# Optimization experiments

Hardware: AMD Instinct MI355X
Metric: run time of the kernel (lower is better)

The kernel has to match this reference:

```python
import jax, jax.numpy as jnp
import numpy as np

B, CIN, H, W = 32, 16, 32, 128
COUT = 128


def _run_direction(x_hwbc, p):
    # x_hwbc: (H, W, B, CIN); scan order is raster (top-to-bottom, left-to-right).
    # Predecessors: dim0 = cell above (previous row), dim1 = cell to the left.
    xi = jnp.einsum('hwbc,oc->hwbo', x_hwbc, p['w_ii'])
    xf = jnp.einsum('hwbc,oc->hwbo', x_hwbc, p['w_if'])
    xg = jnp.einsum('hwbc,oc->hwbo', x_hwbc, p['w_ig'])
    xo = jnp.einsum('hwbc,oc->hwbo', x_hwbc, p['w_io'])
    Wdim, Bdim = x_hwbc.shape[1], x_hwbc.shape[2]
    O = p['w_hi'].shape[0]
    ws0, ws1 = p['ws'][0], p['ws'][1]

    def branch(xi_, xf_, xg_, xo_, c, h):
        i = jax.nn.sigmoid(xi_ + h @ p['w_hi'].T + p['b_i'])
        f = jax.nn.sigmoid(xf_ + h @ p['w_hf'].T + p['b_f'])
        g = jnp.tanh(xg_ + h @ p['w_hg'].T + p['b_g'])
        o = jax.nn.sigmoid(xo_ + h @ p['w_ho'].T + p['b_o'])
        cn = f * c + i * g
        return cn, o * jnp.tanh(cn)

    def col_step(carry, inp):
        c_left, h_left = carry                      # (B, O)
        xi_, xf_, xg_, xo_, c_top, h_top = inp      # each (B, O)
        c0, h0 = branch(xi_, xf_, xg_, xo_, c_top, h_top)   # vertical predecessor
        c1, h1 = branch(xi_, xf_, xg_, xo_, c_left, h_left) # horizontal predecessor
        ct = ws0 * c0 + ws1 * c1 + p['bias']
        ht = ws0 * h0 + ws1 * h1 + p['bias']
        return (ct, ht), (ct, ht)

    def row_step(carry, row):
        c_top, h_top = carry                        # (W, B, O)
        xi_r, xf_r, xg_r, xo_r = row
        z = jnp.zeros((Bdim, O), xi_r.dtype)
        _, (c_row, h_row) = jax.lax.scan(col_step, (z, z), (xi_r, xf_r, xg_r, xo_r, c_top, h_top))
        return (c_row, h_row), h_row

    z_row = jnp.zeros((Wdim, Bdim, O), x_hwbc.dtype)
    _, h_all = jax.lax.scan(row_step, (z_row, z_row), (xi, xf, xg, xo))
    return h_all  # (H, W, B, O)


def _forward(x, w_ii, w_hi, b_i, w_if, w_hf, b_f, w_ig, w_hg, b_g,
             w_io, w_ho, b_o, weighted_sum, bias):
    # Four scan directions realized by flipping the grid (lr_tb, rl_tb, lr_bt, rl_bt).
    x_hwbc = jnp.transpose(x, (2, 3, 0, 1))  # (H, W, B, CIN)
    flips = [(False, False), (False, True), (True, False), (True, True)]
    outs = []
    for d, (fy, fx) in enumerate(flips):
        xd = x_hwbc
        if fy:
            xd = xd[::-1]
        if fx:
            xd = xd[:, ::-1]
        p = {'w_ii': w_ii[d], 'w_hi': w_hi[d], 'b_i': b_i[d],
             'w_if': w_if[d], 'w_hf': w_hf[d], 'b_f': b_f[d],
             'w_ig': w_ig[d], 'w_hg': w_hg[d], 'b_g': b_g[d],
             'w_io': w_io[d], 'w_ho': w_ho[d], 'b_o': b_o[d],
             'ws': weighted_sum[d], 'bias': bias[d]}
        h = _run_direction(xd, p)
        if fy:
            h = h[::-1]
        if fx:
            h = h[:, ::-1]
        outs.append(h)
    h4 = jnp.stack(outs)                      # (4, H, W, B, O)
    return jnp.transpose(h4, (0, 4, 3, 1, 2)) # (4, O, B, H, W)


def setup_inputs() -> dict:
    key = jax.random.key(0)
    ks = jax.random.split(key, 16)
    xw = lambda k: jax.random.normal(k, (4, COUT, CIN), jnp.float32) * 0.05
    hw = lambda k: jax.random.normal(k, (4, COUT, COUT), jnp.float32) * 0.05
    bb = lambda k: jax.random.normal(k, (4, COUT), jnp.float32) * 0.05
    return {
        'x': jax.random.normal(ks[0], (B, CIN, H, W), jnp.float32),
        'w_ii': xw(ks[1]), 'w_hi': hw(ks[2]), 'b_i': bb(ks[3]),
        'w_if': xw(ks[4]), 'w_hf': hw(ks[5]), 'b_f': bb(ks[6]),
        'w_ig': xw(ks[7]), 'w_hg': hw(ks[8]), 'b_g': bb(ks[9]),
        'w_io': xw(ks[10]), 'w_ho': hw(ks[11]), 'b_o': bb(ks[12]),
        'weighted_sum': jax.random.uniform(ks[13], (4, 2), jnp.float32),
        'bias': bb(ks[14]),
    }


def reference(x, w_ii, w_hi, b_i, w_if, w_hf, b_f, w_ig, w_hg, b_g,
              w_io, w_ho, b_o, weighted_sum, bias):
    return _forward(x, w_ii, w_hi, b_i, w_if, w_hf, b_f, w_ig, w_hg, b_g,
                    w_io, w_ho, b_o, weighted_sum, bias)
```

## Files before the change

### kernel.cpp

```cpp
#include <hip/hip_runtime.h>

#define Hh 32
#define Ww 128
#define BB 32
#define CC 16
#define OO 128
#define DEPTH 4
#define SPIN_CAP (1 << 23)
#define FSTRIDE 32

typedef __attribute__((ext_vector_type(8))) short short8;
typedef __attribute__((ext_vector_type(4))) float f32x4;

__device__ inline short f2bf(float f) {
    unsigned u = __builtin_bit_cast(unsigned, f);
    unsigned r = (u + 0x7FFFu + ((u >> 16) & 1u)) >> 16;
    return (short)r;
}
__device__ inline float bf2f(short s) {
    unsigned u = ((unsigned)(unsigned short)s) << 16;
    return __builtin_bit_cast(float, u);
}
__device__ inline float rcp_(float x) { return __builtin_amdgcn_rcpf(x); }
__device__ inline float sigm(float x) {
    return rcp_(1.f + __builtin_amdgcn_exp2f(-1.442695041f * x));
}
__device__ inline float tanh_(float x) {
    return 1.f - 2.f * rcp_(__builtin_amdgcn_exp2f(2.885390082f * x) + 1.f);
}

__device__ inline unsigned long long aload64(const unsigned long long* p) {
    return __hip_atomic_load(p, __ATOMIC_RELAXED, __HIP_MEMORY_SCOPE_AGENT);
}
__device__ inline void astore64(unsigned long long* p, unsigned long long v) {
    __hip_atomic_store(p, v, __ATOMIC_RELAXED, __HIP_MEMORY_SCOPE_AGENT);
}
__device__ inline short aloadS(const short* p) {
    return __hip_atomic_load(p, __ATOMIC_RELAXED, __HIP_MEMORY_SCOPE_AGENT);
}
__device__ inline int aloadI(const int* p) {
    return __hip_atomic_load(p, __ATOMIC_RELAXED, __HIP_MEMORY_SCOPE_AGENT);
}
__device__ inline void astoreI(int* p, int v) {
    __hip_atomic_store(p, v, __ATOMIC_RELAXED, __HIP_MEMORY_SCOPE_AGENT);
}

__global__ void mdlstm_init(const float* __restrict__ x, short* __restrict__ xT,
                            int* __restrict__ flags) {
    int idx = blockIdx.x * 256 + threadIdx.x;
    if (blockIdx.x < 64) flags[idx] = 0;
    int w = idx & 127;
    int h = (idx >> 7) & 31;
    int c = (idx >> 12) & 15;
    int b = idx >> 16;
    float v = x[idx];
    xT[((h * Ww + w) * BB + b) * CC + c] = f2bf(v);
}

__global__ void __launch_bounds__(512, 1) mdlstm_main(
    const short* __restrict__ xT,
    const float* __restrict__ w_ii, const float* __restrict__ w_hi, const float* __restrict__ b_i,
    const float* __restrict__ w_if, const float* __restrict__ w_hf, const float* __restrict__ b_f,
    const float* __restrict__ w_ig, const float* __restrict__ w_hg, const float* __restrict__ b_g,
    const float* __restrict__ w_io, const float* __restrict__ w_ho, const float* __restrict__ b_o,
    const float* __restrict__ wsum, const float* __restrict__ bias,
    short* __restrict__ hring, float* __restrict__ cring,
    int* __restrict__ prog, int* __restrict__ cons,
    float* __restrict__ out)
{
    const int chain = blockIdx.x & 7;
    const int r     = blockIdx.x >> 3;
    const int d     = chain >> 1;
    const int s     = chain & 1;
    const int b0    = s * 16;
    const bool fy   = (d >= 2);
    const bool fx   = (d & 1);
    const int hh    = fy ? (Hh - 1 - r) : r;

    const int tid  = threadIdx.x;
    const int wv   = tid >> 6;
    const int lane = tid & 63;
    const int lr   = lane & 15;
    const int lh   = lane >> 4;
    const int on   = wv * 16 + lr;

    __shared__ short stage[OO * 256];

    const float* whp[4] = {w_hi, w_hf, w_hg, w_ho};
    const float* wip[4] = {w_ii, w_if, w_ig, w_io};
    short8 whf[4][4];
    short8 wif_[4];
#pragma unroll
    for (int g = 0; g < 4; ++g) {
#pragma unroll
        for (int kt = 0; kt < 4; ++kt) {
            const float* p = whp[g] + ((d * OO + on) * OO + kt * 32 + lh * 8);
            short8 f;
#pragma unroll
            for (int j = 0; j < 8; ++j) f[j] = f2bf(p[j]);
            whf[g][kt] = f;
        }
        short8 fi = (short8)(short)0;
        if (lh < 2) {
            const float* p = wip[g] + ((d * OO + on) * CC + lh * 8);
#pragma unroll
            for (int j = 0; j < 8; ++j) fi[j] = f2bf(p[j]);
        }
        wif_[g] = fi;
    }

    const float bi  = b_i[d * OO + on];
    const float bf_ = b_f[d * OO + on];
    const float bg_ = b_g[d * OO + on];
    const float bo_ = b_o[d * OO + on];
    const float bb_ = bias[d * OO + on];
    const float ws0 = wsum[d * 2 + 0];
    const float ws1 = wsum[d * 2 + 1];

    int* topf      = prog + ((d * 32 + (r - 1)) * 2 + s) * FSTRIDE;
    int* myprog    = prog + ((d * 32 + r) * 2 + s) * FSTRIDE;
    int* mycons    = cons + ((d * 32 + r) * 2 + s) * FSTRIDE;
    int* consnext  = cons + ((d * 32 + (r + 1)) * 2 + s) * FSTRIDE;

    const int rb_me  = (d * 32 + r) * DEPTH * BB * OO;
    const int rb_top = (d * 32 + (r - 1)) * DEPTH * BB * OO;

    short8 hLf[4];
#pragma unroll
    for (int kt = 0; kt < 4; ++kt) hLf[kt] = (short8)(short)0;
    float cL[4] = {0.f, 0.f, 0.f, 0.f};

    short8 hTfB[4];
#pragma unroll
    for (int kt = 0; kt < 4; ++kt) hTfB[kt] = (short8)(short)0;
    float cTB[4] = {0.f, 0.f, 0.f, 0.f};

    int top_seen = 0, cons_seen = 0;
    const f32x4 zacc = {0.f, 0.f, 0.f, 0.f};

#pragma unroll 2
    for (int wsc = 0; wsc < Ww; ++wsc) {
        const int ww    = fx ? (Ww - 1 - wsc) : wsc;
        const int slot  = wsc & (DEPTH - 1);
        const int wslot = ww & 15;
        const bool evenc = ((wsc & 1) == 0);

        short8 xf = (short8)(short)0;
        if (lh < 2) {
            const short* p = xT + ((hh * Ww + ww) * BB + b0 + lr) * CC + lh * 8;
            xf = *(const short8*)p;
        }

        short8 hTf[4];
        float cT[4];
        if (r > 0) {
            if (evenc) {
                const int need = wsc + 2;
                if (top_seen < need) {
                    int spin = 0;
                    while (top_seen < need && spin < SPIN_CAP) {
                        int v = 0;
                        if (lane == 0) v = aloadI(topf);
                        v = __shfl(v, 0, 64);
                        if (v < need) { __builtin_amdgcn_s_sleep(1); ++spin; } else top_seen = v;
                    }
                }
                const short* hb = hring + rb_top + slot * OO * BB + b0 + lr;
#pragma unroll
                for (int kt = 0; kt < 4; ++kt) {
                    short8 f;
#pragma unroll
                    for (int jj = 0; jj < 8; ++jj)
                        f[jj] = aloadS(hb + (kt * 32 + lh * 8 + jj) * BB);
                    hTf[kt] = f;
                }
                const short* hb2 = hb + OO * BB;
#pragma unroll
                for (int kt = 0; kt < 4; ++kt) {
                    short8 f;
#pragma unroll
                    for (int jj = 0; jj < 8; ++jj)
                        f[jj] = aloadS(hb2 + (kt * 32 + lh * 8 + jj) * BB);
                    hTfB[kt] = f;
                }
                const unsigned long long* cp =
                    (const unsigned long long*)(cring + rb_top + slot * OO * BB + on * BB + b0 + lh * 4);
                union { unsigned long long q; float f[2]; } c01, c23;
                c01.q = aload64(cp);
                c23.q = aload64(cp + 1);
                cT[0] = c01.f[0]; cT[1] = c01.f[1]; cT[2] = c23.f[0]; cT[3] = c23.f[1];
                const unsigned long long* cp2 = cp + (OO * BB / 2);
                c01.q = aload64(cp2);
                c23.q = aload64(cp2 + 1);
                cTB[0] = c01.f[0]; cTB[1] = c01.f[1]; cTB[2] = c23.f[0]; cTB[3] = c23.f[1];
            } else {
#pragma unroll
                for (int kt = 0; kt < 4; ++kt) hTf[kt] = hTfB[kt];
#pragma unroll
                for (int j = 0; j < 4; ++j) cT[j] = cTB[j];
            }
        } else {
#pragma unroll
            for (int kt = 0; kt < 4; ++kt) hTf[kt] = (short8)(short)0;
#pragma unroll
            for (int j = 0; j < 4; ++j) cT[j] = 0.f;
        }

        f32x4 ax[4], accL[4], accT[4];
#pragma unroll
        for (int g = 0; g < 4; ++g)
            ax[g] = __builtin_amdgcn_mfma_f32_16x16x32_bf16(xf, wif_[g], zacc, 0, 0, 0);
#pragma unroll
        for (int g = 0; g < 4; ++g) {
            f32x4 a = ax[g];
#pragma unroll
            for (int kt = 0; kt < 4; ++kt)
                a = __builtin_amdgcn_mfma_f32_16x16x32_bf16(hLf[kt], whf[g][kt], a, 0, 0, 0);
            accL[g] = a;
        }
#pragma unroll
        for (int g = 0; g < 4; ++g) {
            f32x4 a = ax[g];
#pragma unroll
            for (int kt = 0; kt < 4; ++kt)
                a = __builtin_amdgcn_mfma_f32_16x16x32_bf16(hTf[kt], whf[g][kt], a, 0, 0, 0);
            accT[g] = a;
        }

        float ctv[4];
        union { short sh[4]; unsigned long long q; } hpack;
#pragma unroll
        for (int j = 0; j < 4; ++j) {
            float iT = sigm(accT[0][j] + bi);
            float fT = sigm(accT[1][j] + bf_);
            float gT = tanh_(accT[2][j] + bg_);
            float oT = sigm(accT[3][j] + bo_);
            float c0 = fT * cT[j] + iT * gT;
            float h0 = oT * tanh_(c0);

            float iL = sigm(accL[0][j] + bi);
            float fL = sigm(accL[1][j] + bf_);
            float gL = tanh_(accL[2][j] + bg_);
            float oL = sigm(accL[3][j] + bo_);
            float c1 = fL * cL[j] + iL * gL;
            float h1 = oL * tanh_(c1);

            float ct = ws0 * c0 + ws1 * c1 + bb_;
            float ht = ws0 * h0 + ws1 * h1 + bb_;
            cL[j] = ct;
            ctv[j] = ct;
            hpack.sh[j] = f2bf(ht);
        }

        {
            const int g_on = (on >> 3) & 15;
            *(unsigned long long*)&stage[on * 256 + ((wslot ^ g_on) << 4) + lh * 4] = hpack.q;
        }

        if (r < 31 && evenc && wsc >= DEPTH) {
            const int need = wsc - 2;
            if (cons_seen < need) {
                int spin = 0;
                while (cons_seen < need && spin < SPIN_CAP) {
                    int v = 0;
                    if (lane == 0) v = aloadI(consnext);
                    v = __shfl(v, 0, 64);
                    if (v < need) { __builtin_amdgcn_s_sleep(1); ++spin; } else cons_seen = v;
                }
            }
        }

        if (r < 31) {
            astore64((unsigned long long*)(hring + rb_me + slot * OO * BB + on * BB + b0 + lh * 4),
                     hpack.q);
            union { float f[2]; unsigned long long q; } p01, p23;
            p01.f[0] = ctv[0]; p01.f[1] = ctv[1];
            p23.f[0] = ctv[2]; p23.f[1] = ctv[3];
            unsigned long long* cp =
                (unsigned long long*)(cring + rb_me + slot * OO * BB + on * BB + b0 + lh * 4);
            astore64(cp, p01.q);
            astore64(cp + 1, p23.q);
        }

        __syncthreads();

        if (!evenc && tid == 0) {
            if (r < 31) astoreI(myprog, wsc + 1);
            if (r > 0)  astoreI(mycons, wsc + 1);
        }

        if (r > 0 && !evenc && wsc < Ww - 1) {
            int v = 0;
            if (lane == 0) v = aloadI(topf);
            v = __shfl(v, 0, 64);
            if (v > top_seen) top_seen = v;
        }

#pragma unroll
        for (int kt = 0; kt < 4; ++kt) {
            const int col = ((wslot ^ (kt * 4 + lh)) << 4) + lr;
            short8 f;
#pragma unroll
            for (int jj = 0; jj < 8; ++jj)
                f[jj] = stage[(kt * 32 + lh * 8 + jj) * 256 + col];
            hLf[kt] = f;
        }

        if ((wsc & 15) == 15) {
            const int wbase = ww & ~15;
            const int q  = tid & 3;
            const int r0 = tid >> 2;
#pragma unroll
            for (int i = 0; i < 16; ++i) {
                const int row = r0 + (i << 7);
                const int o = row >> 4;
                const int b = row & 15;
                const int go = (o >> 3) & 15;
                f32x4 v;
#pragma unroll
                for (int k = 0; k < 4; ++k)
                    v[k] = bf2f(stage[o * 256 + (((q * 4 + k) ^ go) << 4) + b]);
                float* op = out + ((size_t)((d * OO + o) * BB + b0 + b)) * (Hh * Ww)
                                + hh * Ww + wbase + q * 4;
                *(f32x4*)op = v;
            }
            __syncthreads();
        }
    }
}

extern "C" void kernel_launch(void* const* d_in, const int* in_sizes, int n_in,
                              void* d_out, int out_size, void* d_ws, size_t ws_size,
                              hipStream_t stream) {
    (void)in_sizes; (void)n_in; (void)out_size; (void)ws_size;

    const float* x     = (const float*)d_in[0];
    const float* w_ii  = (const float*)d_in[1];
    const float* w_hi  = (const float*)d_in[2];
    const float* b_i   = (const float*)d_in[3];
    const float* w_if  = (const float*)d_in[4];
    const float* w_hf  = (const float*)d_in[5];
    const float* b_f   = (const float*)d_in[6];
    const float* w_ig  = (const float*)d_in[7];
    const float* w_hg  = (const float*)d_in[8];
    const float* b_g   = (const float*)d_in[9];
    const float* w_io  = (const float*)d_in[10];
    const float* w_ho  = (const float*)d_in[11];
    const float* b_o   = (const float*)d_in[12];
    const float* wsum  = (const float*)d_in[13];
    const float* bias  = (const float*)d_in[14];
    float* outp        = (float*)d_out;

    char* ws = (char*)d_ws;
    int*   flags  = (int*)ws;
    short* xTp    = (short*)(ws + (64u << 10));
    short* hringp = (short*)(ws + (64u << 10) + (4u << 20));
    float* cringp = (float*)(ws + (64u << 10) + (8u << 20));
    int*   progp  = flags;
    int*   consp  = flags + 256 * FSTRIDE;

    hipLaunchKernelGGL(mdlstm_init, dim3(8192), dim3(256), 0, stream, x, xTp, flags);

    mdlstm_main<<<dim3(256), dim3(512), 0, stream>>>(
        xTp,
        w_ii, w_hi, b_i,
        w_if, w_hf, b_f,
        w_ig, w_hg, b_g,
        w_io, w_ho, b_o,
        wsum, bias,
        hringp, cringp, progp, consp,
        outp);
}
```

Measured before the change: 1.107 ms.

## Relayout h/c rings per batch-half, deepen ring, vectorize top-row reads

```diff
diff --git a/kernel.cpp b/kernel.cpp
--- a/kernel.cpp
+++ b/kernel.cpp
@@ -5,7 +5,6 @@
 #define BB 32
 #define CC 16
 #define OO 128
-#define DEPTH 4
 #define SPIN_CAP (1 << 23)
 #define FSTRIDE 32
 
@@ -35,8 +34,8 @@
 __device__ inline void astore64(unsigned long long* p, unsigned long long v) {
     __hip_atomic_store(p, v, __ATOMIC_RELAXED, __HIP_MEMORY_SCOPE_AGENT);
 }
-__device__ inline short aloadS(const short* p) {
-    return __hip_atomic_load(p, __ATOMIC_RELAXED, __HIP_MEMORY_SCOPE_AGENT);
+__device__ inline void astore16(short* p, short v) {
+    __hip_atomic_store(p, v, __ATOMIC_RELAXED, __HIP_MEMORY_SCOPE_AGENT);
 }
 __device__ inline int aloadI(const int* p) {
     return __hip_atomic_load(p, __ATOMIC_RELAXED, __HIP_MEMORY_SCOPE_AGENT);
@@ -66,7 +65,7 @@
     const float* __restrict__ wsum, const float* __restrict__ bias,
     short* __restrict__ hring, float* __restrict__ cring,
     int* __restrict__ prog, int* __restrict__ cons,
-    float* __restrict__ out)
+    float* __restrict__ out, int depth)
 {
     const int chain = blockIdx.x & 7;
     const int r     = blockIdx.x >> 3;
@@ -122,8 +121,11 @@
     int* mycons    = cons + ((d * 32 + r) * 2 + s) * FSTRIDE;
     int* consnext  = cons + ((d * 32 + (r + 1)) * 2 + s) * FSTRIDE;
 
-    const int rb_me  = (d * 32 + r) * DEPTH * BB * OO;
-    const int rb_top = (d * 32 + (r - 1)) * DEPTH * BB * OO;
+    const int rbh_me  = ((d * 32 + r)     * 2 + s) * depth * (16 * OO);
+    const int rbh_top = ((d * 32 + (r-1)) * 2 + s) * depth * (16 * OO);
+    const int rbc_me  = ((d * 32 + r)     * 2 + s) * depth * (OO * 16);
+    const int rbc_top = ((d * 32 + (r-1)) * 2 + s) * depth * (OO * 16);
+    const int smask   = depth - 1;
 
     short8 hLf[4];
 #pragma unroll
@@ -141,14 +143,14 @@
 #pragma unroll 2
     for (int wsc = 0; wsc < Ww; ++wsc) {
         const int ww    = fx ? (Ww - 1 - wsc) : wsc;
-        const int slot  = wsc & (DEPTH - 1);
+        const int slot  = wsc & smask;
         const int wslot = ww & 15;
         const bool evenc = ((wsc & 1) == 0);
 
         short8 xf = (short8)(short)0;
         if (lh < 2) {
-            const short* p = xT + ((hh * Ww + ww) * BB + b0 + lr) * CC + lh * 8;
-            xf = *(const short8*)p;
+            const short8* p = (const short8*)(xT + ((hh * Ww + ww) * BB + b0 + lr) * CC + lh * 8);
+            xf = __builtin_nontemporal_load(p);
         }
 
         short8 hTf[4];
@@ -165,33 +167,35 @@
                         if (v < need) { __builtin_amdgcn_s_sleep(1); ++spin; } else top_seen = v;
                     }
                 }
-                const short* hb = hring + rb_top + slot * OO * BB + b0 + lr;
+                const short* hb = hring + rbh_top + slot * (16 * OO) + lr * OO;
 #pragma unroll
                 for (int kt = 0; kt < 4; ++kt) {
-                    short8 f;
-#pragma unroll
-                    for (int jj = 0; jj < 8; ++jj)
-                        f[jj] = aloadS(hb + (kt * 32 + lh * 8 + jj) * BB);
-                    hTf[kt] = f;
+                    union { unsigned long long q; short8 v8; } u, u2;
+                    u.q = aload64((const unsigned long long*)(hb + kt * 32 + lh * 8));
+                    (void)u2;
+                    union { unsigned long long q[2]; short8 v; } w;
+                    w.q[0] = aload64((const unsigned long long*)(hb + kt * 32 + lh * 8));
+                    w.q[1] = aload64((const unsigned long long*)(hb + kt * 32 + lh * 8 + 4));
+                    hTf[kt] = w.v;
                 }
-                const short* hb2 = hb + OO * BB;
+                const short* hb2 = hb + 16 * OO;
 #pragma unroll
                 for (int kt = 0; kt < 4; ++kt) {
-                    short8 f;
-#pragma unroll
-                    for (int jj = 0; jj < 8; ++jj)
-                        f[jj] = aloadS(hb2 + (kt * 32 + lh * 8 + jj) * BB);
-                    hTfB[kt] = f;
+                    union { unsigned long long q[2]; short8 v; } w;
+                    w.q[0] = aload64((const unsigned long long*)(hb2 + kt * 32 + lh * 8));
+                    w.q[1] = aload64((const unsigned long long*)(hb2 + kt * 32 + lh * 8 + 4));
+                    hTfB[kt] = w.v;
                 }
                 const unsigned long long* cp =
-                    (const unsigned long long*)(cring + rb_top + slot * OO * BB + on * BB + b0 + lh * 4);
+                    (const unsigned long long*)(cring + rbc_top + slot * (OO * 16) + on * 16 + lh * 4);
                 union { unsigned long long q; float f[2]; } c01, c23;
                 c01.q = aload64(cp);
                 c23.q = aload64(cp + 1);
                 cT[0] = c01.f[0]; cT[1] = c01.f[1]; cT[2] = c23.f[0]; cT[3] = c23.f[1];
-                const unsigned long long* cp2 = cp + (OO * BB / 2);
-                c01.q = aload64(cp2);
-                c23.q = aload64(cp2 + 1);
+                const unsigned long long* cpB =
+                    (const unsigned long long*)(cring + rbc_top + (slot + 1) * (OO * 16) + on * 16 + lh * 4);
+                c01.q = aload64(cpB);
+                c23.q = aload64(cpB + 1);
                 cTB[0] = c01.f[0]; cTB[1] = c01.f[1]; cTB[2] = c23.f[0]; cTB[3] = c23.f[1];
             } else {
 #pragma unroll
@@ -257,8 +261,8 @@
             *(unsigned long long*)&stage[on * 256 + ((wslot ^ g_on) << 4) + lh * 4] = hpack.q;
         }
 
-        if (r < 31 && evenc && wsc >= DEPTH) {
-            const int need = wsc - 2;
+        if (r < 31 && evenc && wsc >= depth) {
+            const int need = wsc - (depth - 2);
             if (cons_seen < need) {
                 int spin = 0;
                 while (cons_seen < need && spin < SPIN_CAP) {
@@ -271,13 +275,15 @@
         }
 
         if (r < 31) {
-            astore64((unsigned long long*)(hring + rb_me + slot * OO * BB + on * BB + b0 + lh * 4),
-                     hpack.q);
+            short* hp = hring + rbh_me + slot * (16 * OO) + on;
+#pragma unroll
+            for (int j = 0; j < 4; ++j)
+                astore16(hp + (lh * 4 + j) * OO, hpack.sh[j]);
             union { float f[2]; unsigned long long q; } p01, p23;
             p01.f[0] = ctv[0]; p01.f[1] = ctv[1];
             p23.f[0] = ctv[2]; p23.f[1] = ctv[3];
             unsigned long long* cp =
-                (unsigned long long*)(cring + rb_me + slot * OO * BB + on * BB + b0 + lh * 4);
+                (unsigned long long*)(cring + rbc_me + slot * (OO * 16) + on * 16 + lh * 4);
             astore64(cp, p01.q);
             astore64(cp + 1, p23.q);
         }
@@ -322,7 +328,7 @@
                     v[k] = bf2f(stage[o * 256 + (((q * 4 + k) ^ go) << 4) + b]);
                 float* op = out + ((size_t)((d * OO + o) * BB + b0 + b)) * (Hh * Ww)
                                 + hh * Ww + wbase + q * 4;
-                *(f32x4*)op = v;
+                __builtin_nontemporal_store(v, (f32x4*)op);
             }
             __syncthreads();
         }
@@ -332,7 +338,7 @@
 extern "C" void kernel_launch(void* const* d_in, const int* in_sizes, int n_in,
                               void* d_out, int out_size, void* d_ws, size_t ws_size,
                               hipStream_t stream) {
-    (void)in_sizes; (void)n_in; (void)out_size; (void)ws_size;
+    (void)in_sizes; (void)n_in; (void)out_size;
 
     const float* x     = (const float*)d_in[0];
     const float* w_ii  = (const float*)d_in[1];
@@ -354,8 +360,14 @@
     char* ws = (char*)d_ws;
     int*   flags  = (int*)ws;
     short* xTp    = (short*)(ws + (64u << 10));
-    short* hringp = (short*)(ws + (64u << 10) + (4u << 20));
-    float* cringp = (float*)(ws + (64u << 10) + (8u << 20));
+    const size_t off_h = (64u << 10) + (4u << 20);
+
+    int depth = 8;
+    const size_t need8 = off_h + ((size_t)8 << 20) + ((size_t)16 << 20) + (1u << 20);
+    if (ws_size < need8) depth = 4;
+
+    short* hringp = (short*)(ws + off_h);
+    float* cringp = (float*)(ws + off_h + ((size_t)depth << 20));
     int*   progp  = flags;
     int*   consp  = flags + 256 * FSTRIDE;
 
@@ -369,5 +381,5 @@
         w_io, w_ho, b_o,
         wsum, bias,
         hringp, cringp, progp, consp,
-        outp);
-}
+        outp, depth);
+}
```

New measurement: 1.249 ms. 1.13x slower.
